# Kernel optimization log

Hardware: AMD Instinct MI355X
Metric: run time of the kernel (lower is better)

The kernel has to match this reference:

```python
import jax, jax.numpy as jnp
import numpy as np

# ---- Haar DWT (levels=1, mode='zero'), matches pytorch_wavelets ordering ----
# For even H,W and filter length 2, zero-pad haar analysis reduces to
# non-overlapping 2x2 blocks. Subband order after the two 1D analyses
# (width first, then height): LL, (w-lo,h-hi), (w-hi,h-lo), HH.

def haar_dwt(x):
    a = x[..., 0::2, 0::2]
    b = x[..., 0::2, 1::2]
    c = x[..., 1::2, 0::2]
    d = x[..., 1::2, 1::2]
    ll = (a + b + c + d) * 0.5
    h0 = (a + b - c - d) * 0.5   # lo-width, hi-height
    h1 = (a - b + c - d) * 0.5   # hi-width, lo-height
    hh = (a - b - c + d) * 0.5
    return ll, jnp.stack([h0, h1, hh], axis=2)  # yh: (b,c,3,h/2,w/2)


def _interleave(u, v, axis):
    # interleave two equal-shaped arrays along `axis` (negative axis)
    s = list(u.shape)
    s[axis] *= 2
    return jnp.stack([u, v], axis=axis + len(u.shape) + 1).reshape(s)


def haar_idwt(ll, yh):
    h0, h1, hh = yh[:, :, 0], yh[:, :, 1], yh[:, :, 2]
    a = (ll + h0 + h1 + hh) * 0.5
    b = (ll + h0 - h1 - hh) * 0.5
    c = (ll - h0 + h1 - hh) * 0.5
    d = (ll - h0 - h1 + hh) * 0.5
    top = _interleave(a, b, -1)   # even rows
    bot = _interleave(c, d, -1)   # odd rows
    return _interleave(top, bot, -2)


def batched_dynamic_conv(feat, kernels, pad):
    """feat: (b,cin,h,w), kernels: (b,cout,cin,kh,kw) -> (b,cout,h,w).
    Per-sample kernels via grouped conv (batch as groups)."""
    bsz, cin, h, w = feat.shape
    cout, kh, kw = kernels.shape[1], kernels.shape[3], kernels.shape[4]
    lhs = feat.reshape(1, bsz * cin, h, w)
    rhs = kernels.reshape(bsz * cout, cin, kh, kw)
    out = jax.lax.conv_general_dilated(
        lhs, rhs, window_strides=(1, 1), padding=[(pad, pad), (pad, pad)],
        dimension_numbers=('NCHW', 'OIHW', 'NCHW'), feature_group_count=bsz)
    return out.reshape(bsz, cout, h, w)


def _dyn_conv_subband(feat, sub_kernels, attn_w, attn_b, pad=1):
    # attention: 1x1 conv -> global avg pool -> softmax over kernel_num
    logits = jnp.einsum('bchw,kc->bk', feat, attn_w) / (feat.shape[-2] * feat.shape[-1]) + attn_b
    att = jax.nn.softmax(logits, axis=1)                       # (b,K)
    kernels = jnp.einsum('bk,koiuv->boiuv', att, sub_kernels)  # (b,cout,cin,kh,kw)
    return batched_dynamic_conv(feat, kernels, pad)


def setup_inputs() -> dict:
    key = jax.random.key(0)
    k1, k2, k3, k4 = jax.random.split(key, 4)
    B, C, H, W = 8, 64, 128, 128
    K, SUB, COUT, KS = 4, 4, 64, 3  # kernel_num, 1+3*levels, out_channels, kernel_size
    return {
        'x': jax.random.normal(k1, (B, C, H, W), dtype=jnp.float32),
        'wt_kernels': jax.random.normal(k2, (K, SUB, COUT, C, KS, KS), dtype=jnp.float32) * 0.02,
        'attn_w': jax.random.normal(k3, (K, C), dtype=jnp.float32) * 0.1,
        'attn_b': jnp.zeros((K,), dtype=jnp.float32),
    }


def reference(x, wt_kernels, attn_w, attn_b):
    ll, yh = haar_dwt(x)
    subbands = [ll, yh[:, :, 0], yh[:, :, 1], yh[:, :, 2]]
    outs = [_dyn_conv_subband(sb, wt_kernels[:, i], attn_w, attn_b, pad=1)
            for i, sb in enumerate(subbands)]
    rec_yh = jnp.stack(outs[1:4], axis=2)  # (b,cout,3,h/2,w/2)
    return haar_idwt(outs[0], rec_yh)
```

## Files before the change

### kernel.cpp

```cpp
#include <hip/hip_runtime.h>
#include <hip/hip_bf16.h>
#include <math.h>


typedef __bf16 bf16x8 __attribute__((ext_vector_type(8)));
typedef float f32x4 __attribute__((ext_vector_type(4)));

__device__ __forceinline__ bf16x8 as_bf16x8(uint4 u) {
    union { uint4 a; bf16x8 b; } c; c.a = u; return c.b;
}
__device__ __forceinline__ unsigned short bf16bits(float f) {
    __hip_bfloat16 h = __float2bfloat16(f);
    union { __hip_bfloat16 h; unsigned short u; } c; c.h = h; return c.u;
}

__global__ __launch_bounds__(256)
void dwt_kernel(const float* __restrict__ x, unsigned short* __restrict__ feats,
                float* __restrict__ sums) {
    __shared__ uint4 sT[2304];
    unsigned short* sTu = (unsigned short*)sT;
    int y = blockIdx.x, b = blockIdx.y;
    int t = threadIdx.x;
    int c = t >> 2, q = t & 3;

    const float4* r0 = (const float4*)x + ((size_t)(b * 64 + c) * 128 + 2 * y) * 32;
    const float4* r1 = r0 + 32;

    float s0 = 0.f, s1 = 0.f, s2 = 0.f, s3 = 0.f;
    #pragma unroll
    for (int i = 0; i < 8; ++i) {
        int f = i * 4 + q;
        float4 p = r0[f], qq = r1[f];
        int xo = 2 * f;
        {
            float a = p.x, bb = p.y, cc = qq.x, dd = qq.y;
            float ll = (a + bb + cc + dd) * 0.5f, h0 = (a + bb - cc - dd) * 0.5f;
            float h1 = (a - bb + cc - dd) * 0.5f, hh = (a - bb - cc + dd) * 0.5f;
            s0 += ll; s1 += h0; s2 += h1; s3 += hh;
            sTu[0 * 4608 + xo * 72 + c] = bf16bits(ll);
            sTu[1 * 4608 + xo * 72 + c] = bf16bits(h0);
            sTu[2 * 4608 + xo * 72 + c] = bf16bits(h1);
            sTu[3 * 4608 + xo * 72 + c] = bf16bits(hh);
        }
        {
            float a = p.z, bb = p.w, cc = qq.z, dd = qq.w;
            float ll = (a + bb + cc + dd) * 0.5f, h0 = (a + bb - cc - dd) * 0.5f;
            float h1 = (a - bb + cc - dd) * 0.5f, hh = (a - bb - cc + dd) * 0.5f;
            s0 += ll; s1 += h0; s2 += h1; s3 += hh;
            sTu[0 * 4608 + (xo + 1) * 72 + c] = bf16bits(ll);
            sTu[1 * 4608 + (xo + 1) * 72 + c] = bf16bits(h0);
            sTu[2 * 4608 + (xo + 1) * 72 + c] = bf16bits(h1);
            sTu[3 * 4608 + (xo + 1) * 72 + c] = bf16bits(hh);
        }
    }
    s0 += __shfl_xor(s0, 1); s0 += __shfl_xor(s0, 2);
    s1 += __shfl_xor(s1, 1); s1 += __shfl_xor(s1, 2);
    s2 += __shfl_xor(s2, 1); s2 += __shfl_xor(s2, 2);
    s3 += __shfl_xor(s3, 1); s3 += __shfl_xor(s3, 2);
    if (q == 0) {
        float* sp = sums + (size_t)(b * 64 + c) * 4;
        atomicAdd(sp + 0, s0); atomicAdd(sp + 1, s1);
        atomicAdd(sp + 2, s2); atomicAdd(sp + 3, s3);
    }
    __syncthreads();
    uint4* fch = (uint4*)feats;
    for (int e = t; e < 2048; e += 256) {
        int s = e >> 9, xx = (e >> 3) & 63, ck = e & 7;
        fch[(size_t)((b * 4 + s) * 64 + y) * 512 + xx * 8 + ck] = sT[s * 576 + xx * 9 + ck];
    }
}

__global__ __launch_bounds__(256)
void mix_kernel(const float* __restrict__ wt, const float* __restrict__ attn_w,
                const float* __restrict__ attn_b, const float* __restrict__ sums,
                unsigned short* __restrict__ wmix) {
    __shared__ float sLw[4][576];
    __shared__ float satt[8][4];
    int co = blockIdx.x, sub = blockIdx.y;
    int t = threadIdx.x;

    if (t < 32) {
        int b = t >> 2, k = t & 3;
        float acc = 0.f;
        #pragma unroll 8
        for (int c = 0; c < 64; ++c)
            acc += attn_w[k * 64 + c] * sums[((size_t)(b * 64 + c) << 2) + sub];
        float logit = acc * (1.0f / 4096.0f) + attn_b[k];
        float m = fmaxf(logit, __shfl_xor(logit, 1));
        m = fmaxf(m, __shfl_xor(m, 2));
        float e = expf(logit - m);
        float s = e + __shfl_xor(e, 1);
        s += __shfl_xor(s, 2);
        satt[b][k] = e / s;
    }
    for (int e = t; e < 2304; e += 256) {
        int k = e / 576, r = e - k * 576;
        sLw[k][r] = wt[((size_t)(k * 4 + sub) * 64 + co) * 576 + r];
    }
    __syncthreads();
    #pragma unroll
    for (int j = 0; j < 18; ++j) {
        int idx = j * 256 + t;
        int b = idx / 576;
        int r = idx - b * 576;
        int tap = r >> 6, ci = r & 63;
        int wi = ci * 9 + tap;
        float v = satt[b][0] * sLw[0][wi] + satt[b][1] * sLw[1][wi]
                + satt[b][2] * sLw[2][wi] + satt[b][3] * sLw[3][wi];
        wmix[((size_t)(b * 4 + sub) * 9 + tap) * 4096 + co * 64 + ci] = bf16bits(v);
    }
}

__global__ __launch_bounds__(256, 2)
void conv_kernel(const unsigned short* __restrict__ feats,
                 const unsigned short* __restrict__ wmix,
                 unsigned short* __restrict__ conv_out) {
    __shared__ uint4 sA[1296];
    __shared__ uint4 sW[2304];
    int tile = blockIdx.x, sub = blockIdx.y, b = blockIdx.z;
    int y0 = (tile >> 2) * 16, x0 = (tile & 3) * 16;
    int t = threadIdx.x, w = t >> 6, l = t & 63;
    int l16 = l & 15, kg = l >> 4;
    const uint4* fch = (const uint4*)feats + (size_t)(b * 4 + sub) * 32768;
    const uint4* wch = (const uint4*)wmix + (size_t)(b * 4 + sub) * 4608;

    f32x4 acc[4][4];
    #pragma unroll
    for (int r = 0; r < 4; ++r)
        #pragma unroll
        for (int nn = 0; nn < 4; ++nn)
            acc[r][nn] = (f32x4){0.f, 0.f, 0.f, 0.f};

    #pragma unroll
    for (int ck8 = 0; ck8 < 8; ck8 += 4) {
        __syncthreads();
        for (int e = t; e < 1296; e += 256) {
            int py = e / 72, rr = e - py * 72, px = rr >> 2, g = rr & 3;
            int gy = y0 - 1 + py, gx = x0 - 1 + px;
            uint4 v = make_uint4(0u, 0u, 0u, 0u);
            if ((unsigned)gy < 64u && (unsigned)gx < 64u)
                v = fch[(gy * 64 + gx) * 8 + ck8 + g];
            sA[e] = v;
        }
        for (int e = t; e < 2304; e += 256) {
            int tap = e >> 8, co = (e >> 2) & 63, g = e & 3;
            sW[e] = wch[tap * 512 + co * 8 + ck8 + g];
        }
        __syncthreads();
        #pragma unroll
        for (int tap = 0; tap < 9; ++tap) {
            int dy = tap / 3, dx = tap - dy * 3;
            bf16x8 bfr[4];
            #pragma unroll
            for (int nn = 0; nn < 4; ++nn)
                bfr[nn] = as_bf16x8(sW[tap * 256 + (nn * 16 + l16) * 4 + kg]);
            #pragma unroll
            for (int r = 0; r < 4; ++r) {
                bf16x8 af = as_bf16x8(sA[((w * 4 + r + dy) * 18 + l16 + dx) * 4 + kg]);
                #pragma unroll
                for (int nn = 0; nn < 4; ++nn)
                    acc[r][nn] = __builtin_amdgcn_mfma_f32_16x16x32_bf16(
                        af, bfr[nn], acc[r][nn], 0, 0, 0);
            }
        }
    }
    size_t obase = (size_t)(b * 4 + sub) * 262144;
    #pragma unroll
    for (int r = 0; r < 4; ++r) {
        int yy = y0 + w * 4 + r;
        #pragma unroll
        for (int nn = 0; nn < 4; ++nn) {
            int co = nn * 16 + l16;
            #pragma unroll
            for (int j = 0; j < 4; ++j) {
                int xx = x0 + kg * 4 + j;
                conv_out[obase + ((size_t)yy * 64 + xx) * 64 + co] = bf16bits(acc[r][nn][j]);
            }
        }
    }
}

__global__ __launch_bounds__(256)
void idwt_kernel(const unsigned short* __restrict__ conv_out,
                 float* __restrict__ out) {
    __shared__ uint4 sT[2304];
    int y = blockIdx.x, b = blockIdx.y;
    int t = threadIdx.x;
    const uint4* cch = (const uint4*)conv_out;
    for (int e = t; e < 2048; e += 256) {
        int s = e >> 9, xx = (e >> 3) & 63, ck = e & 7;
        sT[s * 576 + xx * 9 + ck] = cch[(size_t)(b * 4 + s) * 32768 + y * 512 + xx * 8 + ck];
    }
    __syncthreads();
    int xx = t & 63, cw = t >> 6;
    #pragma unroll
    for (int half = 0; half < 2; ++half) {
        int ckk = half * 4 + cw;
        bf16x8 v0 = as_bf16x8(sT[0 * 576 + xx * 9 + ckk]);
        bf16x8 v1 = as_bf16x8(sT[1 * 576 + xx * 9 + ckk]);
        bf16x8 v2 = as_bf16x8(sT[2 * 576 + xx * 9 + ckk]);
        bf16x8 v3 = as_bf16x8(sT[3 * 576 + xx * 9 + ckk]);
        #pragma unroll
        for (int j = 0; j < 8; ++j) {
            int c = ckk * 8 + j;
            float ll = (float)v0[j], h0 = (float)v1[j];
            float h1 = (float)v2[j], hh = (float)v3[j];
            float a = (ll + h0 + h1 + hh) * 0.5f;
            float bb = (ll + h0 - h1 - hh) * 0.5f;
            float cc = (ll - h0 + h1 - hh) * 0.5f;
            float dd = (ll - h0 - h1 + hh) * 0.5f;
            float2* o0 = (float2*)out + ((size_t)(b * 64 + c) * 128 + 2 * y) * 64 + xx;
            o0[0]  = make_float2(a, bb);
            o0[64] = make_float2(cc, dd);
        }
    }
}

extern "C" void kernel_launch(void* const* d_in, const int* in_sizes, int n_in,
                              void* d_out, int out_size, void* d_ws, size_t ws_size,
                              hipStream_t stream) {
    const float* x  = (const float*)d_in[0];
    const float* wt = (const float*)d_in[1];
    const float* aw = (const float*)d_in[2];
    const float* ab = (const float*)d_in[3];
    float* out = (float*)d_out;
    char* ws = (char*)d_ws;

    float* sums              = (float*)ws;
    unsigned short* feats    = (unsigned short*)(ws + 8192);
    unsigned short* wmix     = (unsigned short*)(ws + 8192 + 16777216);
    unsigned short* conv_out = (unsigned short*)(ws + 8192 + 16777216 + 2359296);

    hipMemsetAsync(sums, 0, 8192, stream);
    hipLaunchKernelGGL(dwt_kernel, dim3(64, 8), dim3(256), 0, stream, x, feats, sums);
    hipLaunchKernelGGL(mix_kernel, dim3(64, 4), dim3(256), 0, stream, wt, aw, ab, sums, wmix);
    hipLaunchKernelGGL(conv_kernel, dim3(16, 4, 8), dim3(256), 0, stream, feats, wmix, conv_out);
    hipLaunchKernelGGL(idwt_kernel, dim3(64, 8), dim3(256), 0, stream, conv_out, out);
}
```

Measured before the change: 134.4 us.

## Fuse inverse DWT into conv kernel and replace atomics with per-row logits

```diff
diff --git a/kernel.cpp b/kernel.cpp
--- a/kernel.cpp
+++ b/kernel.cpp
@@ -15,9 +15,10 @@
 }
 
 __global__ __launch_bounds__(256)
-void dwt_kernel(const float* __restrict__ x, unsigned short* __restrict__ feats,
-                float* __restrict__ sums) {
+void dwt_kernel(const float* __restrict__ x, const float* __restrict__ attn_w,
+                unsigned short* __restrict__ feats, float* __restrict__ plog) {
     __shared__ uint4 sT[2304];
+    __shared__ float sred[64][4];
     unsigned short* sTu = (unsigned short*)sT;
     int y = blockIdx.x, b = blockIdx.y;
     int t = threadIdx.x;
@@ -57,12 +58,16 @@
     s1 += __shfl_xor(s1, 1); s1 += __shfl_xor(s1, 2);
     s2 += __shfl_xor(s2, 1); s2 += __shfl_xor(s2, 2);
     s3 += __shfl_xor(s3, 1); s3 += __shfl_xor(s3, 2);
-    if (q == 0) {
-        float* sp = sums + (size_t)(b * 64 + c) * 4;
-        atomicAdd(sp + 0, s0); atomicAdd(sp + 1, s1);
-        atomicAdd(sp + 2, s2); atomicAdd(sp + 3, s3);
-    }
+    if (q == 0) { sred[c][0] = s0; sred[c][1] = s1; sred[c][2] = s2; sred[c][3] = s3; }
     __syncthreads();
+    if (t < 16) {
+        int sub = t >> 2, k = t & 3;
+        float acc = 0.f;
+        #pragma unroll 8
+        for (int cc = 0; cc < 64; ++cc)
+            acc += attn_w[k * 64 + cc] * sred[cc][sub];
+        plog[((size_t)(b * 4 + sub) * 4 + k) * 64 + y] = acc;
+    }
     uint4* fch = (uint4*)feats;
     for (int e = t; e < 2048; e += 256) {
         int s = e >> 9, xx = (e >> 3) & 63, ck = e & 7;
@@ -71,9 +76,8 @@
 }
 
 __global__ __launch_bounds__(256)
-void mix_kernel(const float* __restrict__ wt, const float* __restrict__ attn_w,
-                const float* __restrict__ attn_b, const float* __restrict__ sums,
-                unsigned short* __restrict__ wmix) {
+void mix_kernel(const float* __restrict__ wt, const float* __restrict__ attn_b,
+                const float* __restrict__ plog, unsigned short* __restrict__ wmix) {
     __shared__ float sLw[4][576];
     __shared__ float satt[8][4];
     int co = blockIdx.x, sub = blockIdx.y;
@@ -81,10 +85,10 @@
 
     if (t < 32) {
         int b = t >> 2, k = t & 3;
+        const float* pp = plog + ((size_t)(b * 4 + sub) * 4 + k) * 64;
         float acc = 0.f;
         #pragma unroll 8
-        for (int c = 0; c < 64; ++c)
-            acc += attn_w[k * 64 + c] * sums[((size_t)(b * 64 + c) << 2) + sub];
+        for (int yy = 0; yy < 64; ++yy) acc += pp[yy];
         float logit = acc * (1.0f / 4096.0f) + attn_b[k];
         float m = fmaxf(logit, __shfl_xor(logit, 1));
         m = fmaxf(m, __shfl_xor(m, 2));
@@ -112,107 +116,101 @@
 }
 
 __global__ __launch_bounds__(256, 2)
-void conv_kernel(const unsigned short* __restrict__ feats,
-                 const unsigned short* __restrict__ wmix,
-                 unsigned short* __restrict__ conv_out) {
-    __shared__ uint4 sA[1296];
-    __shared__ uint4 sW[2304];
-    int tile = blockIdx.x, sub = blockIdx.y, b = blockIdx.z;
+void conv_idwt_kernel(const unsigned short* __restrict__ feats,
+                      const unsigned short* __restrict__ wmix,
+                      float* __restrict__ out) {
+    __shared__ uint4 sA[2592];
+    __shared__ uint4 sW[1152];
+    int cg = blockIdx.x, tile = blockIdx.y, b = blockIdx.z;
     int y0 = (tile >> 2) * 16, x0 = (tile & 3) * 16;
     int t = threadIdx.x, w = t >> 6, l = t & 63;
     int l16 = l & 15, kg = l >> 4;
-    const uint4* fch = (const uint4*)feats + (size_t)(b * 4 + sub) * 32768;
-    const uint4* wch = (const uint4*)wmix + (size_t)(b * 4 + sub) * 4608;
+    int w4 = w * 4;
+    const uint4* fchb = (const uint4*)feats + (size_t)b * 131072;
+    const uint4* wchb = (const uint4*)wmix + (size_t)b * 18432;
 
     f32x4 acc[4][4];
     #pragma unroll
-    for (int r = 0; r < 4; ++r)
+    for (int s = 0; s < 4; ++s)
         #pragma unroll
-        for (int nn = 0; nn < 4; ++nn)
-            acc[r][nn] = (f32x4){0.f, 0.f, 0.f, 0.f};
-
-    #pragma unroll
-    for (int ck8 = 0; ck8 < 8; ck8 += 4) {
-        __syncthreads();
-        for (int e = t; e < 1296; e += 256) {
-            int py = e / 72, rr = e - py * 72, px = rr >> 2, g = rr & 3;
-            int gy = y0 - 1 + py, gx = x0 - 1 + px;
-            uint4 v = make_uint4(0u, 0u, 0u, 0u);
-            if ((unsigned)gy < 64u && (unsigned)gx < 64u)
-                v = fch[(gy * 64 + gx) * 8 + ck8 + g];
-            sA[e] = v;
-        }
-        for (int e = t; e < 2304; e += 256) {
-            int tap = e >> 8, co = (e >> 2) & 63, g = e & 3;
-            sW[e] = wch[tap * 512 + co * 8 + ck8 + g];
-        }
-        __syncthreads();
+        for (int r = 0; r < 4; ++r)
+            acc[s][r] = (f32x4){0.f, 0.f, 0.f, 0.f};
+
+    #pragma unroll
+    for (int sp = 0; sp < 2; ++sp) {
         #pragma unroll
-        for (int tap = 0; tap < 9; ++tap) {
-            int dy = tap / 3, dx = tap - dy * 3;
-            bf16x8 bfr[4];
+        for (int ck8 = 0; ck8 < 8; ck8 += 4) {
+            __syncthreads();
+            for (int e = t; e < 2592; e += 256) {
+                int s2 = e / 1296, rr = e - s2 * 1296;
+                int py = rr / 72, r2 = rr - py * 72, px = r2 >> 2, g = r2 & 3;
+                int gy = y0 - 1 + py, gx = x0 - 1 + px;
+                uint4 v = make_uint4(0u, 0u, 0u, 0u);
+                if ((unsigned)gy < 64u && (unsigned)gx < 64u)
+                    v = fchb[(size_t)(sp * 2 + s2) * 32768 + (gy * 64 + gx) * 8 + ck8 + g];
+                sA[e] = v;
+            }
+            for (int e = t; e < 1152; e += 256) {
+                int s2 = e / 576, r = e - s2 * 576;
+                int tap = r >> 6, co = (r >> 2) & 15, g = r & 3;
+                sW[e] = wchb[(size_t)(sp * 2 + s2) * 4608 + tap * 512
+                             + (cg * 16 + co) * 8 + ck8 + g];
+            }
+            __syncthreads();
             #pragma unroll
-            for (int nn = 0; nn < 4; ++nn)
-                bfr[nn] = as_bf16x8(sW[tap * 256 + (nn * 16 + l16) * 4 + kg]);
-            #pragma unroll
-            for (int r = 0; r < 4; ++r) {
-                bf16x8 af = as_bf16x8(sA[((w * 4 + r + dy) * 18 + l16 + dx) * 4 + kg]);
+            for (int s2 = 0; s2 < 2; ++s2) {
+                int s = sp * 2 + s2;
+                int abase = s2 * 1296;
+                uint4 af[4][3];
                 #pragma unroll
-                for (int nn = 0; nn < 4; ++nn)
-                    acc[r][nn] = __builtin_amdgcn_mfma_f32_16x16x32_bf16(
-                        af, bfr[nn], acc[r][nn], 0, 0, 0);
+                for (int i = 0; i < 4; ++i)
+                    #pragma unroll
+                    for (int dx = 0; dx < 3; ++dx)
+                        af[i][dx] = sA[abase + ((w4 + i) * 18 + l16 + dx) * 4 + kg];
+                #pragma unroll
+                for (int dy = 0; dy < 3; ++dy) {
+                    if (dy > 0) {
+                        #pragma unroll
+                        for (int i = 0; i < 3; ++i)
+                            #pragma unroll
+                            for (int dx = 0; dx < 3; ++dx)
+                                af[i][dx] = af[i + 1][dx];
+                        #pragma unroll
+                        for (int dx = 0; dx < 3; ++dx)
+                            af[3][dx] = sA[abase + ((w4 + dy + 3) * 18 + l16 + dx) * 4 + kg];
+                    }
+                    #pragma unroll
+                    for (int dx = 0; dx < 3; ++dx) {
+                        uint4 bw = sW[s2 * 576 + (dy * 3 + dx) * 64 + l16 * 4 + kg];
+                        bf16x8 bfr = as_bf16x8(bw);
+                        #pragma unroll
+                        for (int r = 0; r < 4; ++r)
+                            acc[s][r] = __builtin_amdgcn_mfma_f32_16x16x32_bf16(
+                                as_bf16x8(af[r][dx]), bfr, acc[s][r], 0, 0, 0);
+                    }
+                }
             }
         }
     }
-    size_t obase = (size_t)(b * 4 + sub) * 262144;
+    int co = cg * 16 + l16;
     #pragma unroll
     for (int r = 0; r < 4; ++r) {
-        int yy = y0 + w * 4 + r;
+        int ys = y0 + w4 + r;
+        float* orow = out + ((size_t)(b * 64 + co) * 128 + 2 * ys) * 128 + 2 * x0 + 8 * kg;
+        float av[4], bv[4], cv[4], dv[4];
         #pragma unroll
-        for (int nn = 0; nn < 4; ++nn) {
-            int co = nn * 16 + l16;
-            #pragma unroll
-            for (int j = 0; j < 4; ++j) {
-                int xx = x0 + kg * 4 + j;
-                conv_out[obase + ((size_t)yy * 64 + xx) * 64 + co] = bf16bits(acc[r][nn][j]);
-            }
-        }
-    }
-}
-
-__global__ __launch_bounds__(256)
-void idwt_kernel(const unsigned short* __restrict__ conv_out,
-                 float* __restrict__ out) {
-    __shared__ uint4 sT[2304];
-    int y = blockIdx.x, b = blockIdx.y;
-    int t = threadIdx.x;
-    const uint4* cch = (const uint4*)conv_out;
-    for (int e = t; e < 2048; e += 256) {
-        int s = e >> 9, xx = (e >> 3) & 63, ck = e & 7;
-        sT[s * 576 + xx * 9 + ck] = cch[(size_t)(b * 4 + s) * 32768 + y * 512 + xx * 8 + ck];
-    }
-    __syncthreads();
-    int xx = t & 63, cw = t >> 6;
-    #pragma unroll
-    for (int half = 0; half < 2; ++half) {
-        int ckk = half * 4 + cw;
-        bf16x8 v0 = as_bf16x8(sT[0 * 576 + xx * 9 + ckk]);
-        bf16x8 v1 = as_bf16x8(sT[1 * 576 + xx * 9 + ckk]);
-        bf16x8 v2 = as_bf16x8(sT[2 * 576 + xx * 9 + ckk]);
-        bf16x8 v3 = as_bf16x8(sT[3 * 576 + xx * 9 + ckk]);
-        #pragma unroll
-        for (int j = 0; j < 8; ++j) {
-            int c = ckk * 8 + j;
-            float ll = (float)v0[j], h0 = (float)v1[j];
-            float h1 = (float)v2[j], hh = (float)v3[j];
-            float a = (ll + h0 + h1 + hh) * 0.5f;
-            float bb = (ll + h0 - h1 - hh) * 0.5f;
-            float cc = (ll - h0 + h1 - hh) * 0.5f;
-            float dd = (ll - h0 - h1 + hh) * 0.5f;
-            float2* o0 = (float2*)out + ((size_t)(b * 64 + c) * 128 + 2 * y) * 64 + xx;
-            o0[0]  = make_float2(a, bb);
-            o0[64] = make_float2(cc, dd);
-        }
+        for (int j = 0; j < 4; ++j) {
+            float ll = acc[0][r][j], h0 = acc[1][r][j];
+            float h1 = acc[2][r][j], hh = acc[3][r][j];
+            av[j] = (ll + h0 + h1 + hh) * 0.5f;
+            bv[j] = (ll + h0 - h1 - hh) * 0.5f;
+            cv[j] = (ll - h0 + h1 - hh) * 0.5f;
+            dv[j] = (ll - h0 - h1 + hh) * 0.5f;
+        }
+        *(float4*)(orow)           = make_float4(av[0], bv[0], av[1], bv[1]);
+        *(float4*)(orow + 4)       = make_float4(av[2], bv[2], av[3], bv[3]);
+        *(float4*)(orow + 128)     = make_float4(cv[0], dv[0], cv[1], dv[1]);
+        *(float4*)(orow + 132)     = make_float4(cv[2], dv[2], cv[3], dv[3]);
     }
 }
 
@@ -226,14 +224,12 @@
     float* out = (float*)d_out;
     char* ws = (char*)d_ws;
 
-    float* sums              = (float*)ws;
-    unsigned short* feats    = (unsigned short*)(ws + 8192);
-    unsigned short* wmix     = (unsigned short*)(ws + 8192 + 16777216);
-    unsigned short* conv_out = (unsigned short*)(ws + 8192 + 16777216 + 2359296);
-
-    hipMemsetAsync(sums, 0, 8192, stream);
-    hipLaunchKernelGGL(dwt_kernel, dim3(64, 8), dim3(256), 0, stream, x, feats, sums);
-    hipLaunchKernelGGL(mix_kernel, dim3(64, 4), dim3(256), 0, stream, wt, aw, ab, sums, wmix);
-    hipLaunchKernelGGL(conv_kernel, dim3(16, 4, 8), dim3(256), 0, stream, feats, wmix, conv_out);
-    hipLaunchKernelGGL(idwt_kernel, dim3(64, 8), dim3(256), 0, stream, conv_out, out);
-}
+    float* plog              = (float*)ws;
+    unsigned short* feats    = (unsigned short*)(ws + 32768);
+    unsigned short* wmix     = (unsigned short*)(ws + 32768 + 16777216);
+
+    hipLaunchKernelGGL(dwt_kernel, dim3(64, 8), dim3(256), 0, stream, x, aw, feats, plog);
+    hipLaunchKernelGGL(mix_kernel, dim3(64, 4), dim3(256), 0, stream, wt, ab, plog, wmix);
+    hipLaunchKernelGGL(conv_idwt_kernel, dim3(4, 16, 8), dim3(256), 0, stream,
+                       feats, wmix, out);
+}
```

New measurement: 133.5 us. Within noise of the previous version (-0.7%).

## Split conv output channels across blocks and replace atomics with per-row partial logits

Applied to the files above, without the earlier changes.

```diff
diff --git a/kernel.cpp b/kernel.cpp
--- a/kernel.cpp
+++ b/kernel.cpp
@@ -15,9 +15,10 @@
 }
 
 __global__ __launch_bounds__(256)
-void dwt_kernel(const float* __restrict__ x, unsigned short* __restrict__ feats,
-                float* __restrict__ sums) {
+void dwt_kernel(const float* __restrict__ x, const float* __restrict__ attn_w,
+                unsigned short* __restrict__ feats, float* __restrict__ plog) {
     __shared__ uint4 sT[2304];
+    __shared__ float sred[64][4];
     unsigned short* sTu = (unsigned short*)sT;
     int y = blockIdx.x, b = blockIdx.y;
     int t = threadIdx.x;
@@ -57,12 +58,16 @@
     s1 += __shfl_xor(s1, 1); s1 += __shfl_xor(s1, 2);
     s2 += __shfl_xor(s2, 1); s2 += __shfl_xor(s2, 2);
     s3 += __shfl_xor(s3, 1); s3 += __shfl_xor(s3, 2);
-    if (q == 0) {
-        float* sp = sums + (size_t)(b * 64 + c) * 4;
-        atomicAdd(sp + 0, s0); atomicAdd(sp + 1, s1);
-        atomicAdd(sp + 2, s2); atomicAdd(sp + 3, s3);
-    }
+    if (q == 0) { sred[c][0] = s0; sred[c][1] = s1; sred[c][2] = s2; sred[c][3] = s3; }
     __syncthreads();
+    if (t < 16) {
+        int sub = t >> 2, k = t & 3;
+        float acc = 0.f;
+        #pragma unroll 8
+        for (int cc = 0; cc < 64; ++cc)
+            acc += attn_w[k * 64 + cc] * sred[cc][sub];
+        plog[((size_t)(b * 4 + sub) * 4 + k) * 64 + y] = acc;
+    }
     uint4* fch = (uint4*)feats;
     for (int e = t; e < 2048; e += 256) {
         int s = e >> 9, xx = (e >> 3) & 63, ck = e & 7;
@@ -71,9 +76,8 @@
 }
 
 __global__ __launch_bounds__(256)
-void mix_kernel(const float* __restrict__ wt, const float* __restrict__ attn_w,
-                const float* __restrict__ attn_b, const float* __restrict__ sums,
-                unsigned short* __restrict__ wmix) {
+void mix_kernel(const float* __restrict__ wt, const float* __restrict__ attn_b,
+                const float* __restrict__ plog, unsigned short* __restrict__ wmix) {
     __shared__ float sLw[4][576];
     __shared__ float satt[8][4];
     int co = blockIdx.x, sub = blockIdx.y;
@@ -81,10 +85,10 @@
 
     if (t < 32) {
         int b = t >> 2, k = t & 3;
+        const float* pp = plog + ((size_t)(b * 4 + sub) * 4 + k) * 64;
         float acc = 0.f;
         #pragma unroll 8
-        for (int c = 0; c < 64; ++c)
-            acc += attn_w[k * 64 + c] * sums[((size_t)(b * 64 + c) << 2) + sub];
+        for (int yy = 0; yy < 64; ++yy) acc += pp[yy];
         float logit = acc * (1.0f / 4096.0f) + attn_b[k];
         float m = fmaxf(logit, __shfl_xor(logit, 1));
         m = fmaxf(m, __shfl_xor(m, 2));
@@ -111,25 +115,28 @@
     }
 }
 
-__global__ __launch_bounds__(256, 2)
+__global__ __launch_bounds__(256, 4)
 void conv_kernel(const unsigned short* __restrict__ feats,
                  const unsigned short* __restrict__ wmix,
                  unsigned short* __restrict__ conv_out) {
     __shared__ uint4 sA[1296];
-    __shared__ uint4 sW[2304];
-    int tile = blockIdx.x, sub = blockIdx.y, b = blockIdx.z;
+    __shared__ uint4 sW[1152];
+    int bx = blockIdx.x;
+    int tile = bx & 15, cg = bx >> 4;
+    int sub = blockIdx.y, b = blockIdx.z;
     int y0 = (tile >> 2) * 16, x0 = (tile & 3) * 16;
     int t = threadIdx.x, w = t >> 6, l = t & 63;
     int l16 = l & 15, kg = l >> 4;
+    int w4 = w * 4;
     const uint4* fch = (const uint4*)feats + (size_t)(b * 4 + sub) * 32768;
     const uint4* wch = (const uint4*)wmix + (size_t)(b * 4 + sub) * 4608;
 
-    f32x4 acc[4][4];
-    #pragma unroll
-    for (int r = 0; r < 4; ++r)
-        #pragma unroll
-        for (int nn = 0; nn < 4; ++nn)
-            acc[r][nn] = (f32x4){0.f, 0.f, 0.f, 0.f};
+    f32x4 acc[4][2];
+    #pragma unroll
+    for (int r = 0; r < 4; ++r) {
+        acc[r][0] = (f32x4){0.f, 0.f, 0.f, 0.f};
+        acc[r][1] = (f32x4){0.f, 0.f, 0.f, 0.f};
+    }
 
     #pragma unroll
     for (int ck8 = 0; ck8 < 8; ck8 += 4) {
@@ -142,35 +149,51 @@
                 v = fch[(gy * 64 + gx) * 8 + ck8 + g];
             sA[e] = v;
         }
-        for (int e = t; e < 2304; e += 256) {
-            int tap = e >> 8, co = (e >> 2) & 63, g = e & 3;
-            sW[e] = wch[tap * 512 + co * 8 + ck8 + g];
+        for (int e = t; e < 1152; e += 256) {
+            int tap = e >> 7, rr = e & 127, co = rr >> 2, g = rr & 3;
+            sW[e] = wch[tap * 512 + (cg * 32 + co) * 8 + ck8 + g];
         }
         __syncthreads();
-        #pragma unroll
-        for (int tap = 0; tap < 9; ++tap) {
-            int dy = tap / 3, dx = tap - dy * 3;
-            bf16x8 bfr[4];
+        uint4 af[4][3];
+        #pragma unroll
+        for (int i = 0; i < 4; ++i)
             #pragma unroll
-            for (int nn = 0; nn < 4; ++nn)
-                bfr[nn] = as_bf16x8(sW[tap * 256 + (nn * 16 + l16) * 4 + kg]);
+            for (int dx = 0; dx < 3; ++dx)
+                af[i][dx] = sA[((w4 + i) * 18 + l16 + dx) * 4 + kg];
+        #pragma unroll
+        for (int dy = 0; dy < 3; ++dy) {
+            if (dy > 0) {
+                #pragma unroll
+                for (int i = 0; i < 3; ++i)
+                    #pragma unroll
+                    for (int dx = 0; dx < 3; ++dx)
+                        af[i][dx] = af[i + 1][dx];
+                #pragma unroll
+                for (int dx = 0; dx < 3; ++dx)
+                    af[3][dx] = sA[((w4 + dy + 3) * 18 + l16 + dx) * 4 + kg];
+            }
             #pragma unroll
-            for (int r = 0; r < 4; ++r) {
-                bf16x8 af = as_bf16x8(sA[((w * 4 + r + dy) * 18 + l16 + dx) * 4 + kg]);
+            for (int dx = 0; dx < 3; ++dx) {
+                int tap = dy * 3 + dx;
+                bf16x8 bw0 = as_bf16x8(sW[tap * 128 + l16 * 4 + kg]);
+                bf16x8 bw1 = as_bf16x8(sW[tap * 128 + (16 + l16) * 4 + kg]);
                 #pragma unroll
-                for (int nn = 0; nn < 4; ++nn)
-                    acc[r][nn] = __builtin_amdgcn_mfma_f32_16x16x32_bf16(
-                        af, bfr[nn], acc[r][nn], 0, 0, 0);
+                for (int r = 0; r < 4; ++r) {
+                    acc[r][0] = __builtin_amdgcn_mfma_f32_16x16x32_bf16(
+                        as_bf16x8(af[r][dx]), bw0, acc[r][0], 0, 0, 0);
+                    acc[r][1] = __builtin_amdgcn_mfma_f32_16x16x32_bf16(
+                        as_bf16x8(af[r][dx]), bw1, acc[r][1], 0, 0, 0);
+                }
             }
         }
     }
     size_t obase = (size_t)(b * 4 + sub) * 262144;
     #pragma unroll
     for (int r = 0; r < 4; ++r) {
-        int yy = y0 + w * 4 + r;
-        #pragma unroll
-        for (int nn = 0; nn < 4; ++nn) {
-            int co = nn * 16 + l16;
+        int yy = y0 + w4 + r;
+        #pragma unroll
+        for (int nn = 0; nn < 2; ++nn) {
+            int co = cg * 32 + nn * 16 + l16;
             #pragma unroll
             for (int j = 0; j < 4; ++j) {
                 int xx = x0 + kg * 4 + j;
@@ -226,14 +249,14 @@
     float* out = (float*)d_out;
     char* ws = (char*)d_ws;
 
-    float* sums              = (float*)ws;
-    unsigned short* feats    = (unsigned short*)(ws + 8192);
-    unsigned short* wmix     = (unsigned short*)(ws + 8192 + 16777216);
-    unsigned short* conv_out = (unsigned short*)(ws + 8192 + 16777216 + 2359296);
-
-    hipMemsetAsync(sums, 0, 8192, stream);
-    hipLaunchKernelGGL(dwt_kernel, dim3(64, 8), dim3(256), 0, stream, x, feats, sums);
-    hipLaunchKernelGGL(mix_kernel, dim3(64, 4), dim3(256), 0, stream, wt, aw, ab, sums, wmix);
-    hipLaunchKernelGGL(conv_kernel, dim3(16, 4, 8), dim3(256), 0, stream, feats, wmix, conv_out);
+    float* plog              = (float*)ws;
+    unsigned short* feats    = (unsigned short*)(ws + 32768);
+    unsigned short* wmix     = (unsigned short*)(ws + 32768 + 16777216);
+    unsigned short* conv_out = (unsigned short*)(ws + 32768 + 16777216 + 2359296);
+
+    hipLaunchKernelGGL(dwt_kernel, dim3(64, 8), dim3(256), 0, stream, x, aw, feats, plog);
+    hipLaunchKernelGGL(mix_kernel, dim3(64, 4), dim3(256), 0, stream, wt, ab, plog, wmix);
+    hipLaunchKernelGGL(conv_kernel, dim3(32, 4, 8), dim3(256), 0, stream,
+                       feats, wmix, conv_out);
     hipLaunchKernelGGL(idwt_kernel, dim3(64, 8), dim3(256), 0, stream, conv_out, out);
 }
```

Measured after the change: 123.7 us. -8.0%, faster.
